# Performance work log

Hardware: AMD Instinct MI355X
Metric: run time of the kernel (lower is better)

The kernel has to match this reference:

```python
import jax, jax.numpy as jnp
import numpy as np

N, C_IN, C_OUT = 8192, 128, 128
BN_EPS = 1e-5
EDGE_PROB = 0.004  # avg degree ~33


def setup_inputs() -> dict:
    key = jax.random.key(0)
    k1, k2, k3, k4, k5, k6 = jax.random.split(key, 6)
    node_features = jax.random.normal(k1, (N, C_IN), dtype=jnp.float32)
    # binary dense adjacency (rand fill, thresholded to ~avg degree 33)
    adjacency_matrix = (jax.random.uniform(k2, (N, N)) < EDGE_PROB).astype(jnp.float32)
    s = 1.0 / np.sqrt(C_IN)
    W_n = jax.random.uniform(k3, (C_OUT, C_IN), jnp.float32, -s, s)
    b_n = jax.random.uniform(k4, (C_OUT,), jnp.float32, -s, s)
    W_c = jax.random.uniform(k5, (C_OUT, C_IN), jnp.float32, -s, s)
    b_c = jax.random.uniform(k6, (C_OUT,), jnp.float32, -s, s)
    gamma = jnp.ones((C_OUT,), jnp.float32)
    beta = jnp.zeros((C_OUT,), jnp.float32)
    return {"node_features": node_features, "adjacency_matrix": adjacency_matrix,
            "W_n": W_n, "b_n": b_n, "W_c": W_c, "b_c": b_c,
            "gamma": gamma, "beta": beta}


def reference(node_features, adjacency_matrix, W_n, b_n, W_c, b_c, gamma, beta):
    # mean aggregation: degrees from row-sums (as in the torch code), agg = A.T @ X / deg
    deg = adjacency_matrix.sum(axis=1, keepdims=True)          # [N,1]
    deg = jnp.where(deg == 0, jnp.ones_like(deg), deg)
    agg = (adjacency_matrix.T @ node_features) / deg           # [N,C_in]
    h = agg @ W_n.T + b_n + node_features @ W_c.T + b_c        # [N,C_out]
    # BatchNorm1d, training-mode batch stats (biased variance)
    mu = h.mean(axis=0)
    var = ((h - mu) ** 2).mean(axis=0)
    h_norm = (h - mu) * jax.lax.rsqrt(var + BN_EPS)
    return jax.nn.relu(gamma * h_norm + beta)
```

## Files before the change

kernel.cpp:

```cpp
#include <hip/hip_runtime.h>
#include <stdint.h>

#define NN 8192
#define CC 128
#define BN_EPS 1e-5f

__device__ inline unsigned short f2bf(float f) {
    unsigned int u = __float_as_uint(f);
    unsigned int r = (u + 0x7fffu + ((u >> 16) & 1u)) >> 16;
    return (unsigned short)r;
}

__global__ __launch_bounds__(256, 8) void k1a_mask(
        const float* __restrict__ A, unsigned long long* __restrict__ Mt,
        float* __restrict__ deg) {
    __shared__ float dred[4][64];
    const int lane = threadIdx.x & 63;
    const int wave = threadIdx.x >> 6;
    const int task = blockIdx.x * 4 + wave;
    const int band = task >> 6;
    const int i0   = (task & 63) << 7;
    const int j0   = band << 6;

    const uint2* Ap = reinterpret_cast<const uint2*>(A + (size_t)j0 * NN + i0) + lane;
    unsigned long long m0 = 0, m1 = 0;
    float degc = 0.0f;

    #pragma unroll 8
    for (int j = 0; j < 64; ++j) {
        uint2 v = Ap[(size_t)j * (NN / 2)];
        bool n0 = v.x != 0u, n1 = v.y != 0u;
        unsigned long long b0 = __ballot(n0), b1 = __ballot(n1);
        const unsigned long long bit = 1ull << j;
        if (n0) m0 |= bit;
        if (n1) m1 |= bit;
        if (lane == j) degc = (float)(__popcll(b0) + __popcll(b1));
    }

    unsigned long long* p = Mt + (size_t)band * NN + i0 + 2 * lane;
    *reinterpret_cast<ulonglong2*>(p) = make_ulonglong2(m0, m1);

    dred[wave][lane] = degc;
    __syncthreads();
    if (wave == 0) {
        float s = dred[0][lane] + dred[1][lane] + dred[2][lane] + dred[3][lane];
        atomicAdd(&deg[j0 + lane], s);
    }
}

__global__ __launch_bounds__(256, 8) void k1c_gather(
        const unsigned long long* __restrict__ Mt, const float* __restrict__ X,
        const float* __restrict__ deg, float* __restrict__ aggN) {
    __shared__ float red[4][128];
    const int lane = threadIdx.x & 63;
    const int wave = threadIdx.x >> 6;
    const int i = blockIdx.x;

    unsigned long long w = 0;
    if (lane < 32)
        w = Mt[(size_t)(wave * 32 + lane) * NN + i];
    float acc0 = 0.0f, acc1 = 0.0f;

    unsigned long long any = __ballot(w != 0ull);
    while (any) {
        int q = __builtin_ctzll(any); any &= any - 1;
        unsigned long long u = __shfl(w, q);
        const float* Xq = X + (size_t)((wave * 32 + q) * 64) * CC;
        while (u) {
            int b = __builtin_ctzll(u); u &= u - 1;
            const float* xr = Xq + b * CC;
            acc0 += xr[lane];
            acc1 += xr[64 + lane];
        }
    }

    red[wave][lane]      = acc0;
    red[wave][64 + lane] = acc1;
    __syncthreads();
    if (wave == 0) {
        float s0 = red[0][lane]      + red[1][lane]      + red[2][lane]      + red[3][lane];
        float s1 = red[0][64 + lane] + red[1][64 + lane] + red[2][64 + lane] + red[3][64 + lane];
        float d  = deg[i];
        float rd = (d == 0.0f) ? 1.0f : (1.0f / d);
        aggN[(size_t)i * CC + lane]      = s0 * rd;
        aggN[(size_t)i * CC + 64 + lane] = s1 * rd;
    }
}

__global__ __launch_bounds__(256, 2) void k2_gemm(
        const float* __restrict__ aggN, const float* __restrict__ X,
        const float* __restrict__ Wn, const float* __restrict__ bn,
        const float* __restrict__ Wc, const float* __restrict__ bc,
        float* __restrict__ h, float* __restrict__ bsum, float* __restrict__ bsq) {
    __shared__ unsigned int Wp[128 * 128];
    const int tid = threadIdx.x;
    for (int idx = tid * 4; idx < 128 * 128; idx += 1024) {
        float4 wn4 = *reinterpret_cast<const float4*>(Wn + idx);
        float4 wc4 = *reinterpret_cast<const float4*>(Wc + idx);
        int c = idx >> 7, k0 = idx & 127;
        #pragma unroll
        for (int q = 0; q < 4; ++q) {
            unsigned int pk = (unsigned int)f2bf((&wn4.x)[q])
                            | ((unsigned int)f2bf((&wc4.x)[q]) << 16);
            int k = k0 + q;
            Wp[(k * 128 + c) ^ (k & 31)] = pk;
        }
    }
    __syncthreads();
    const int c  = tid & 127;
    const int rg = tid >> 7;
    const int i0 = blockIdx.x * 16 + rg * 8;

    float accN[8], accC[8];
    #pragma unroll
    for (int r = 0; r < 8; ++r) { accN[r] = 0.0f; accC[r] = 0.0f; }

    float4 ar[8], xr[8], an[8], xn[8];

#define LOADK(ab_, xb_, k_) do {                                               \
    _Pragma("unroll")                                                          \
    for (int r = 0; r < 8; ++r) {                                              \
        ab_[r] = *reinterpret_cast<const float4*>(&aggN[(size_t)(i0 + r) * CC + (k_)]); \
        xb_[r] = *reinterpret_cast<const float4*>(&X[(size_t)(i0 + r) * CC + (k_)]);    \
    }                                                                          \
} while (0)

#define COMPK(ab_, xb_, k_) do {                                               \
    _Pragma("unroll")                                                          \
    for (int kk = 0; kk < 4; ++kk) {                                           \
        int kq_ = (k_) + kk;                                                   \
        unsigned int pk_ = Wp[(kq_ * 128 + c) ^ (kq_ & 31)];                   \
        float wn_ = __uint_as_float(pk_ << 16);                                \
        float wc_ = __uint_as_float(pk_ & 0xffff0000u);                        \
        _Pragma("unroll")                                                      \
        for (int r = 0; r < 8; ++r) {                                          \
            accN[r] = fmaf((&ab_[r].x)[kk], wn_, accN[r]);                     \
            accC[r] = fmaf((&xb_[r].x)[kk], wc_, accC[r]);                     \
        }                                                                      \
    }                                                                          \
} while (0)

    LOADK(ar, xr, 0);
    for (int k = 0; k < 128; k += 8) {
        LOADK(an, xn, k + 4);
        COMPK(ar, xr, k);
        if (k + 8 < 128) LOADK(ar, xr, k + 8);
        COMPK(an, xn, k + 4);
    }

    const float bnc = bn[c], bcc = bc[c];
    float sp = 0.0f, sq = 0.0f;
    #pragma unroll
    for (int r = 0; r < 8; ++r) {
        float hv = accN[r] + accC[r] + bnc + bcc;
        h[(size_t)(i0 + r) * CC + c] = hv;
        sp += hv; sq += hv * hv;
    }
    __syncthreads();
    float* red = reinterpret_cast<float*>(Wp);
    red[rg * 128 + c]       = sp;
    red[256 + rg * 128 + c] = sq;
    __syncthreads();
    if (rg == 0) {
        atomicAdd(&bsum[c], red[c] + red[128 + c]);
        atomicAdd(&bsq[c],  red[256 + c] + red[384 + c]);
    }
}

__global__ __launch_bounds__(256) void k4_bn(
        const float* __restrict__ h, const float* __restrict__ bsum,
        const float* __restrict__ bsq, const float* __restrict__ gamma,
        const float* __restrict__ beta, float* __restrict__ out) {
    const int idx = (blockIdx.x * 256 + threadIdx.x) * 4;
    const int c0  = idx & 127;
    float4 hv = *reinterpret_cast<const float4*>(h + idx);
    float4 s4 = *reinterpret_cast<const float4*>(bsum + c0);
    float4 q4 = *reinterpret_cast<const float4*>(bsq + c0);
    float4 g4 = *reinterpret_cast<const float4*>(gamma + c0);
    float4 b4 = *reinterpret_cast<const float4*>(beta + c0);
    const float invN = 1.0f / 8192.0f;
    float4 o;
    const float* hp = &hv.x; const float* sp = &s4.x; const float* qp = &q4.x;
    const float* gp = &g4.x; const float* bp = &b4.x; float* op = &o.x;
    #pragma unroll
    for (int jj = 0; jj < 4; ++jj) {
        float mu  = sp[jj] * invN;
        float var = qp[jj] * invN - mu * mu;
        float sc  = gp[jj] * rsqrtf(var + BN_EPS);
        float v   = (hp[jj] - mu) * sc + bp[jj];
        op[jj] = v > 0.0f ? v : 0.0f;
    }
    *reinterpret_cast<float4*>(out + idx) = o;
}

extern "C" void kernel_launch(void* const* d_in, const int* in_sizes, int n_in,
                              void* d_out, int out_size, void* d_ws, size_t ws_size,
                              hipStream_t stream) {
    const float* X     = (const float*)d_in[0];
    const float* A     = (const float*)d_in[1];
    const float* Wn    = (const float*)d_in[2];
    const float* bn    = (const float*)d_in[3];
    const float* Wc    = (const float*)d_in[4];
    const float* bc    = (const float*)d_in[5];
    const float* gamma = (const float*)d_in[6];
    const float* beta  = (const float*)d_in[7];
    float* out = (float*)d_out;

    char* ws = (char*)d_ws;
    float* deg  = (float*)(ws);
    float* bsum = (float*)(ws + 32768);
    float* bsq  = (float*)(ws + 33280);
    float* aggN = (float*)(ws + 65536);
    unsigned long long* Mt = (unsigned long long*)(ws + 4259840);
    float* h    = (float*)(ws + 4259840);

    hipMemsetAsync(d_ws, 0, 33792, stream);

    k1a_mask  <<<2048, 256, 0, stream>>>(A, Mt, deg);
    k1c_gather<<<8192, 256, 0, stream>>>(Mt, X, deg, aggN);
    k2_gemm   <<<512,  256, 0, stream>>>(aggN, X, Wn, bn, Wc, bc, h, bsum, bsq);
    k4_bn     <<<1024, 256, 0, stream>>>(h, bsum, bsq, gamma, beta, out);
}
```

Measured before the change: 446.0 us.

## Fuse GEMM and BatchNorm via cooperative grid sync to skip h round-trip

```diff
diff --git a/kernel.cpp b/kernel.cpp
--- a/kernel.cpp
+++ b/kernel.cpp
@@ -1,5 +1,8 @@
 #include <hip/hip_runtime.h>
+#include <hip/hip_cooperative_groups.h>
 #include <stdint.h>
+
+namespace cg = cooperative_groups;
 
 #define NN 8192
 #define CC 128
@@ -84,6 +87,101 @@
         float rd = (d == 0.0f) ? 1.0f : (1.0f / d);
         aggN[(size_t)i * CC + lane]      = s0 * rd;
         aggN[(size_t)i * CC + 64 + lane] = s1 * rd;
+    }
+}
+
+__global__ __launch_bounds__(256, 2) void k2k4_fused(
+        const float* __restrict__ aggN, const float* __restrict__ X,
+        const float* __restrict__ Wn, const float* __restrict__ bn,
+        const float* __restrict__ Wc, const float* __restrict__ bc,
+        float* __restrict__ bsum, float* __restrict__ bsq,
+        const float* __restrict__ gamma, const float* __restrict__ beta,
+        float* __restrict__ out) {
+    __shared__ unsigned int Wp[128 * 128];
+    const int tid = threadIdx.x;
+    for (int idx = tid * 4; idx < 128 * 128; idx += 1024) {
+        float4 wn4 = *reinterpret_cast<const float4*>(Wn + idx);
+        float4 wc4 = *reinterpret_cast<const float4*>(Wc + idx);
+        int c = idx >> 7, k0 = idx & 127;
+        #pragma unroll
+        for (int q = 0; q < 4; ++q) {
+            unsigned int pk = (unsigned int)f2bf((&wn4.x)[q])
+                            | ((unsigned int)f2bf((&wc4.x)[q]) << 16);
+            int k = k0 + q;
+            Wp[(k * 128 + c) ^ (k & 31)] = pk;
+        }
+    }
+    __syncthreads();
+    const int c  = tid & 127;
+    const int rg = tid >> 7;
+    const int i0 = blockIdx.x * 16 + rg * 8;
+
+    float accN[8], accC[8];
+    #pragma unroll
+    for (int r = 0; r < 8; ++r) { accN[r] = 0.0f; accC[r] = 0.0f; }
+
+    float4 ar[8], xr[8], an[8], xn[8];
+
+#define LOADK(ab_, xb_, k_) do {                                               \
+    _Pragma("unroll")                                                          \
+    for (int r = 0; r < 8; ++r) {                                              \
+        ab_[r] = *reinterpret_cast<const float4*>(&aggN[(size_t)(i0 + r) * CC + (k_)]); \
+        xb_[r] = *reinterpret_cast<const float4*>(&X[(size_t)(i0 + r) * CC + (k_)]);    \
+    }                                                                          \
+} while (0)
+
+#define COMPK(ab_, xb_, k_) do {                                               \
+    _Pragma("unroll")                                                          \
+    for (int kk = 0; kk < 4; ++kk) {                                           \
+        int kq_ = (k_) + kk;                                                   \
+        unsigned int pk_ = Wp[(kq_ * 128 + c) ^ (kq_ & 31)];                   \
+        float wn_ = __uint_as_float(pk_ << 16);                                \
+        float wc_ = __uint_as_float(pk_ & 0xffff0000u);                        \
+        _Pragma("unroll")                                                      \
+        for (int r = 0; r < 8; ++r) {                                          \
+            accN[r] = fmaf((&ab_[r].x)[kk], wn_, accN[r]);                     \
+            accC[r] = fmaf((&xb_[r].x)[kk], wc_, accC[r]);                     \
+        }                                                                      \
+    }                                                                          \
+} while (0)
+
+    LOADK(ar, xr, 0);
+    for (int k = 0; k < 128; k += 8) {
+        LOADK(an, xn, k + 4);
+        COMPK(ar, xr, k);
+        if (k + 8 < 128) LOADK(ar, xr, k + 8);
+        COMPK(an, xn, k + 4);
+    }
+
+    const float bnc = bn[c], bcc = bc[c];
+    float hv[8];
+    float sp = 0.0f, sq = 0.0f;
+    #pragma unroll
+    for (int r = 0; r < 8; ++r) {
+        hv[r] = accN[r] + accC[r] + bnc + bcc;
+        sp += hv[r]; sq += hv[r] * hv[r];
+    }
+    __syncthreads();
+    float* red = reinterpret_cast<float*>(Wp);
+    red[rg * 128 + c]       = sp;
+    red[256 + rg * 128 + c] = sq;
+    __syncthreads();
+    if (rg == 0) {
+        atomicAdd(&bsum[c], red[c] + red[128 + c]);
+        atomicAdd(&bsq[c],  red[256 + c] + red[384 + c]);
+    }
+
+    cg::this_grid().sync();
+
+    const float invN = 1.0f / 8192.0f;
+    const float mu  = bsum[c] * invN;
+    const float var = bsq[c] * invN - mu * mu;
+    const float sc  = gamma[c] * rsqrtf(var + BN_EPS);
+    const float bt  = beta[c] - mu * sc;
+    #pragma unroll
+    for (int r = 0; r < 8; ++r) {
+        float v = hv[r] * sc + bt;
+        out[(size_t)(i0 + r) * CC + c] = v > 0.0f ? v : 0.0f;
     }
 }
 
@@ -117,29 +215,6 @@
 
     float4 ar[8], xr[8], an[8], xn[8];
 
-#define LOADK(ab_, xb_, k_) do {                                               \
-    _Pragma("unroll")                                                          \
-    for (int r = 0; r < 8; ++r) {                                              \
-        ab_[r] = *reinterpret_cast<const float4*>(&aggN[(size_t)(i0 + r) * CC + (k_)]); \
-        xb_[r] = *reinterpret_cast<const float4*>(&X[(size_t)(i0 + r) * CC + (k_)]);    \
-    }                                                                          \
-} while (0)
-
-#define COMPK(ab_, xb_, k_) do {                                               \
-    _Pragma("unroll")                                                          \
-    for (int kk = 0; kk < 4; ++kk) {                                           \
-        int kq_ = (k_) + kk;                                                   \
-        unsigned int pk_ = Wp[(kq_ * 128 + c) ^ (kq_ & 31)];                   \
-        float wn_ = __uint_as_float(pk_ << 16);                                \
-        float wc_ = __uint_as_float(pk_ & 0xffff0000u);                        \
-        _Pragma("unroll")                                                      \
-        for (int r = 0; r < 8; ++r) {                                          \
-            accN[r] = fmaf((&ab_[r].x)[kk], wn_, accN[r]);                     \
-            accC[r] = fmaf((&xb_[r].x)[kk], wc_, accC[r]);                     \
-        }                                                                      \
-    }                                                                          \
-} while (0)
-
     LOADK(ar, xr, 0);
     for (int k = 0; k < 128; k += 8) {
         LOADK(an, xn, k + 4);
@@ -218,6 +293,15 @@
 
     k1a_mask  <<<2048, 256, 0, stream>>>(A, Mt, deg);
     k1c_gather<<<8192, 256, 0, stream>>>(Mt, X, deg, aggN);
-    k2_gemm   <<<512,  256, 0, stream>>>(aggN, X, Wn, bn, Wc, bc, h, bsum, bsq);
-    k4_bn     <<<1024, 256, 0, stream>>>(h, bsum, bsq, gamma, beta, out);
-}
+
+    void* ka[] = { (void*)&aggN, (void*)&X, (void*)&Wn, (void*)&bn,
+                   (void*)&Wc, (void*)&bc, (void*)&bsum, (void*)&bsq,
+                   (void*)&gamma, (void*)&beta, (void*)&out };
+    hipError_t ce = hipLaunchCooperativeKernel(
+        reinterpret_cast<const void*>(&k2k4_fused), dim3(512), dim3(256),
+        ka, 0, stream);
+    if (ce != hipSuccess) {
+        k2_gemm<<<512,  256, 0, stream>>>(aggN, X, Wn, bn, Wc, bc, h, bsum, bsq);
+        k4_bn  <<<1024, 256, 0, stream>>>(h, bsum, bsq, gamma, beta, out);
+    }
+}
```

New measurement: 500.8 us. +12.3%, slower.
